# Kernel optimization log

Hardware: AMD Instinct MI355X
Metric: run time of the kernel (lower is better)

The kernel has to match this reference:

```python
import jax, jax.numpy as jnp
from jax import lax
import numpy as np

B, H, W, C = 4, 64, 64, 128
L = H * W
DI = 2 * C   # mamba d_inner (expand=2)
NS = 16      # d_state
R = C // 16  # dt_rank
K = 4        # d_conv
S = 4        # scan branches: fwd, bwd, extra1, extra2


def setup_inputs():
    key = jax.random.key(0)
    ks = jax.random.split(key, 20)
    g = lambda i, shape, s=0.02: jax.random.normal(ks[i], shape, jnp.float32) * s
    return {
        "I1": jax.random.normal(ks[0], (B, L, C), jnp.float32),
        "fusion_resi": jax.random.normal(ks[1], (B, L, C), jnp.float32),
        "I2": jax.random.normal(ks[2], (B, L, C), jnp.float32),
        "fusion": jax.random.normal(ks[3], (B, L, C), jnp.float32),
        "ln1_w": jnp.ones((C,)), "ln1_b": jnp.zeros((C,)),
        "ln2_w": jnp.ones((C,)), "ln2_b": jnp.zeros((C,)),
        "ln3_w": jnp.ones((C,)), "ln3_b": jnp.zeros((C,)),
        "sp_w": g(4, (1, 2, 5, 5), 0.1),
        "ca_w1": g(5, (C // 4, C), 0.05),
        "ca_w2": g(6, (C, C // 4), 0.05),
        "dw_w": g(7, (C, 1, 3, 3), 0.1),
        "dw_b": jnp.zeros((C,)),
        "in_proj_w": g(8, (2 * DI, C)),
        "in_proj1_w": g(9, (DI, C)),
        "in_proj2_w": g(10, (DI, C)),
        "conv_w": g(11, (S, DI, K), 0.1),
        "conv_b": jnp.zeros((S, DI)),
        "xproj_w": g(12, (S, R + 2 * NS, DI)),
        "dt_w": g(13, (S, DI, R), 0.1),
        "dt_b": jnp.full((S, DI), -4.6, jnp.float32),  # softplus -> dt ~ 0.01
        "A_log": jnp.broadcast_to(jnp.log(jnp.arange(1, NS + 1, dtype=jnp.float32)), (S, DI, NS)) * 1.0,
        "Dskip": jnp.ones((S, DI)),
        "out_w": g(14, (C, DI)),
        "test_h": H, "test_w": W,
    }


def ln(x, w, b):
    mu = x.mean(-1, keepdims=True)
    xc = x - mu
    v = (xc * xc).mean(-1, keepdims=True)
    return xc / jnp.sqrt(v + 1e-5) * w + b


def sp_att(x, w, h, wd):
    # x: (B, N, C) -> (B, N, 1) spatial attention map
    Bb = x.shape[0]
    m = jnp.concatenate([x.mean(2, keepdims=True), x.max(2, keepdims=True)], 2)
    m = m.transpose(0, 2, 1).reshape(Bb, 2, h, wd)
    o = lax.conv_general_dilated(m, w, (1, 1), [(2, 2), (2, 2)],
                                 dimension_numbers=("NCHW", "OIHW", "NCHW"))
    return jax.nn.sigmoid(o).reshape(Bb, 1, -1).transpose(0, 2, 1)


def mamba_m3(xf, e1, e2, in_proj_w, in_proj1_w, in_proj2_w, conv_w, conv_b,
             xproj_w, dt_w, dt_b, A_log, Dskip, out_w):
    Bb, Ll, _ = xf.shape
    xz = xf @ in_proj_w.T                       # (B,L,2DI)
    x, z = xz[..., :DI], xz[..., DI:]
    # 4 branches: forward, backward (flipped), extra_emb1, extra_emb2
    u = jnp.stack([x, x[:, ::-1], e1 @ in_proj1_w.T, e2 @ in_proj2_w.T], 0)  # (S,B,L,DI)

    def causal_dwconv(xb, w, b):                # xb (B,L,DI)
        xp = jnp.pad(xb.transpose(0, 2, 1), ((0, 0), (0, 0), (K - 1, 0)))
        o = lax.conv_general_dilated(xp, w[:, None, :], (1,), "VALID",
                                     feature_group_count=DI,
                                     dimension_numbers=("NCH", "OIH", "NCH"))
        return (o + b[None, :, None]).transpose(0, 2, 1)

    uc = jax.nn.silu(jax.vmap(causal_dwconv)(u, conv_w, conv_b))        # (S,B,L,DI)
    proj = jnp.einsum("sbld,spd->sblp", uc, xproj_w)
    dt = jax.nn.softplus(jnp.einsum("sblr,sdr->sbld", proj[..., :R], dt_w)
                         + dt_b[:, None, None, :])                      # (S,B,L,DI)
    Bm, Cm = proj[..., R:R + NS], proj[..., R + NS:]                    # (S,B,L,NS)
    A = -jnp.exp(A_log)                                                 # (S,DI,NS)

    def step(h, inp):
        dt_t, B_t, C_t, u_t = inp                                       # (S,B,DI),(S,B,NS),(S,B,NS),(S,B,DI)
        dA = jnp.exp(dt_t[..., None] * A[:, None])                      # (S,B,DI,NS)
        h = h * dA + (dt_t * u_t)[..., None] * B_t[:, :, None, :]
        return h, jnp.einsum("sbdn,sbn->sbd", h, C_t)

    xs = tuple(t.transpose(2, 0, 1, 3) for t in (dt, Bm, Cm, uc))
    h0 = jnp.zeros((S, Bb, DI, NS), xf.dtype)
    _, ys = lax.scan(step, h0, xs)                                      # (L,S,B,DI)
    y = ys.transpose(1, 2, 0, 3) + uc * Dskip[:, None, None, :]         # (S,B,L,DI)
    y_tot = y[0] + y[1][:, ::-1] + y[2] + y[3]
    return (y_tot * jax.nn.silu(z)) @ out_w.T


def reference(I1, fusion_resi, I2, fusion, ln1_w, ln1_b, ln2_w, ln2_b, ln3_w,
              ln3_b, sp_w, ca_w1, ca_w2, dw_w, dw_b, in_proj_w, in_proj1_w,
              in_proj2_w, conv_w, conv_b, xproj_w, dt_w, dt_b, A_log, Dskip,
              out_w, test_h, test_w):
    fusion_resi = fusion + fusion_resi
    fusion = ln(fusion_resi, ln1_w, ln1_b)
    I2 = ln(I2 * sp_att(I2, sp_w, test_h, test_w), ln2_w, ln2_b)
    I1 = ln(I1 * sp_att(I1, sp_w, test_h, test_w), ln3_w, ln3_b)
    # note: original applies norm1/norm2/norm3 a second time here (faithful)
    gf = mamba_m3(ln(fusion, ln1_w, ln1_b), ln(I2, ln2_w, ln2_b),
                  ln(I1, ln3_w, ln3_b), in_proj_w, in_proj1_w, in_proj2_w,
                  conv_w, conv_b, xproj_w, dt_w, dt_b, A_log, Dskip, out_w)
    Bb, _, Cc = gf.shape
    f4 = gf.transpose(0, 2, 1).reshape(Bb, Cc, test_h, test_w)
    # ChannelAttention1 (already returns x*sig) then extra *fusion per source
    fc = lambda v: jnp.maximum(v @ ca_w1.T, 0.0) @ ca_w2.T
    sig = jax.nn.sigmoid(fc(f4.mean((2, 3))) + fc(f4.max((2, 3))))[:, :, None, None]
    f4 = (f4 * sig) * f4
    dw = lax.conv_general_dilated(f4, dw_w, (1, 1), [(1, 1), (1, 1)],
                                  feature_group_count=Cc,
                                  dimension_numbers=("NCHW", "OIHW", "NCHW"))
    dw = dw + dw_b[None, :, None, None]
    out = (dw + f4).reshape(Bb, Cc, -1).transpose(0, 2, 1)
    return out, fusion_resi
```

## Files before the change

kernel.cpp:

```cpp
#include <hip/hip_runtime.h>

#define DEVI __device__ __forceinline__

static constexpr int BB=4, CC=128, LLn=4096, DI=256, NS=16, RR=8, SS=4;
static constexpr int PP = RR + 2*NS;
static constexpr int CT = 32, NCH = LLn/CT;
static constexpr int NCHF = 64;
static constexpr size_t BLC  = (size_t)BB*LLn*CC;
static constexpr size_t BLD  = (size_t)BB*LLn*DI;
static constexpr size_t SBLD = (size_t)SS*BLD;
static constexpr size_t SBLP = (size_t)SS*BB*LLn*PP;

static constexpr int OW_LN1W=0, OW_LN1B=128, OW_LN2W=256, OW_LN2B=384, OW_LN3W=512, OW_LN3B=640,
 OW_SPW=768, OW_CAW1=820, OW_CAW2=4916, OW_DWW=9012, OW_DWB=10164, OW_IPW=10292,
 OW_IP1W=75828, OW_IP2W=108596, OW_CVW=141364, OW_CVB=145460, OW_XPW=146484,
 OW_DTW=187444, OW_DTB=195636, OW_ALOG=196660, OW_DSK=213044, OW_OUTW=214068;
static constexpr int NW_RAW = 246836;
static constexpr int NW_END = 246848;

__constant__ int c_woff[22] = {OW_LN1W,OW_LN1B,OW_LN2W,OW_LN2B,OW_LN3W,OW_LN3B,OW_SPW,OW_CAW1,
 OW_CAW2,OW_DWW,OW_DWB,OW_IPW,OW_IP1W,OW_IP2W,OW_CVW,OW_CVB,OW_XPW,OW_DTW,OW_DTB,OW_ALOG,
 OW_DSK,OW_OUTW};
__constant__ int c_wsz[22]  = {128,128,128,128,128,128,50,4096,4096,1152,128,65536,32768,32768,
 4096,1024,40960,8192,1024,16384,1024,32768};

static constexpr size_t O_XF   = NW_END;
static constexpr size_t O_E1   = O_XF + BLC;
static constexpr size_t O_E2   = O_E1 + BLC;
static constexpr size_t O_Z    = O_E2 + BLC;
static constexpr size_t O_U    = O_Z + BLD;
static constexpr size_t O_UC   = O_U + SBLD;
static constexpr size_t O_PROJ = O_UC + SBLD;
static constexpr size_t O_SDT  = O_PROJ + SBLP;
static constexpr size_t O_H    = O_SDT + (size_t)SS*BB*NCHF*DI;
static constexpr size_t O_M    = O_H + (size_t)SS*BB*NCHF*DI*NS;
static constexpr size_t O_S    = O_M + 2*(size_t)BB*2*LLn;
static constexpr size_t O_GF   = O_S + 2*(size_t)BB*LLn;
static constexpr size_t O_PART = O_GF + BLC;
static constexpr size_t O_SIG  = O_PART + 2*(size_t)BB*32*CC;
static constexpr size_t WS_END = O_SIG + (size_t)BB*CC;

typedef __attribute__((ext_vector_type(8))) short short8v;
typedef __attribute__((ext_vector_type(4))) float f32x4;

DEVI float bfu2f(unsigned short s){ union{unsigned u; float f;} c; c.u = ((unsigned)s)<<16; return c.f; }
DEVI unsigned short f2bfu(float f){ union{float f; unsigned u;} c; c.f=f;
  unsigned r = c.u + 0x7FFFu + ((c.u>>16)&1u); return (unsigned short)(r>>16); }
DEVI float4 bf4(uint2 v){ return make_float4(bfu2f((unsigned short)(v.x&0xFFFFu)), bfu2f((unsigned short)(v.x>>16)),
                                             bfu2f((unsigned short)(v.y&0xFFFFu)), bfu2f((unsigned short)(v.y>>16))); }
DEVI uint2 pk4(float4 v){ uint2 p;
  p.x = (unsigned)f2bfu(v.x) | ((unsigned)f2bfu(v.y)<<16);
  p.y = (unsigned)f2bfu(v.z) | ((unsigned)f2bfu(v.w)<<16); return p; }
DEVI bool bfmode(const void* ln1w){ return *(const unsigned*)ln1w == 0x3F803F80u; }
DEVI float2 ldin2(const void* p, int i, bool isbf){
  if(isbf){ unsigned v = *(const unsigned*)((const unsigned short*)p + i);
    return make_float2(bfu2f((unsigned short)(v & 0xFFFFu)), bfu2f((unsigned short)(v >> 16))); }
  const float* f = (const float*)p + i; return make_float2(f[0], f[1]);
}
DEVI float wsum(float v){
#pragma unroll
  for(int o=32;o;o>>=1) v += __shfl_xor(v,o,64);
  return v; }
DEVI float wmaxr(float v){
#pragma unroll
  for(int o=32;o;o>>=1) v = fmaxf(v, __shfl_xor(v,o,64));
  return v; }
DEVI float sigf(float x){ return 1.f/(1.f+__expf(-x)); }
DEVI float2 ln_wave(float2 x, const float* Wf, int ow, int ob, int lane){
  float mu = wsum(x.x + x.y) * (1.f/(float)CC);
  float dx = x.x - mu, dy = x.y - mu;
  float var = wsum(dx*dx + dy*dy) * (1.f/(float)CC);
  float rs = rsqrtf(var + 1e-5f);
  int c = 2*lane;
  return make_float2(dx*rs*Wf[ow+c] + Wf[ob+c], dy*rs*Wf[ow+c+1] + Wf[ob+c+1]);
}

struct Srcs { const void* p[22]; };

__global__ void k_xwpad(unsigned* __restrict__ xw32){
  int i = blockIdx.x*256 + threadIdx.x;
  xw32[i] = 0u;
}

__global__ void k_wcvt(Srcs s, float* __restrict__ ws,
                       unsigned short* __restrict__ wip, unsigned short* __restrict__ wob,
                       unsigned short* __restrict__ xw){
  bool isbf = bfmode(s.p[0]);
  int idx = blockIdx.x*256 + threadIdx.x;
  if(idx >= NW_RAW) return;
  int t = 0;
  while(t < 21 && idx >= c_woff[t+1]) t++;
  int j = idx - c_woff[t];
  if(j >= c_wsz[t]) return;
  float v = isbf ? bfu2f(((const unsigned short*)s.p[t])[j]) : ((const float*)s.p[t])[j];
  ws[idx] = v;
  if(t==11)      wip[j]         = f2bfu(v);
  else if(t==12) wip[65536+j]   = f2bfu(v);
  else if(t==13) wip[98304+j]   = f2bfu(v);
  else if(t==21) wob[j]         = f2bfu(v);
  else if(t==16){
    int sid = j / 10240, rem = j % 10240;
    xw[((size_t)sid*64 + rem/256)*256 + (rem%256)] = f2bfu(v);
  }
}

__global__ void k_fuse(const void* fus, const void* fres, const void* ln1raw,
                       float* __restrict__ ws, float* __restrict__ outf,
                       unsigned short* __restrict__ xbf){
  bool isbf = bfmode(ln1raw);
  int lane = threadIdx.x & 63, wv = threadIdx.x >> 6;
  int row = blockIdx.x*4 + wv;
  int base = row*CC;
  float2 a = ldin2(fus, base+2*lane, isbf);
  float2 b = ldin2(fres, base+2*lane, isbf);
  float2 fr = make_float2(a.x+b.x, a.y+b.y);
  *(float2*)(outf + BLC + base + 2*lane) = fr;
  float2 y = ln_wave(fr, ws, OW_LN1W, OW_LN1B, lane);
  y = ln_wave(y, ws, OW_LN1W, OW_LN1B, lane);
  unsigned pk = (unsigned)f2bfu(y.x) | ((unsigned)f2bfu(y.y)<<16);
  *(unsigned*)&xbf[base + 2*lane] = pk;
}

__global__ void k_meanmax(const void* I1, const void* I2, const void* ln1raw, float* __restrict__ ws){
  bool isbf = bfmode(ln1raw);
  int lane = threadIdx.x & 63, wv = threadIdx.x >> 6;
  int g = blockIdx.x*4 + wv;
  int ten = g & 1, row = g >> 1;
  const void* src = ten ? I2 : I1;
  float2 x = ldin2(src, row*CC + 2*lane, isbf);
  float sm = wsum(x.x + x.y) * (1.f/(float)CC);
  float mx = wmaxr(fmaxf(x.x, x.y));
  if(lane == 0){
    int b = row >> 12, l = row & 4095;
    float* mt = ws + O_M + (size_t)ten*(BB*2*LLn);
    mt[(size_t)b*2*LLn + l] = sm;
    mt[(size_t)b*2*LLn + LLn + l] = mx;
  }
}

__global__ void k_spconv(float* __restrict__ ws){
  int idx = blockIdx.x*256 + threadIdx.x;
  int ten = idx >> 14, b = (idx>>12)&3, l = idx & 4095;
  int h = l >> 6, w = l & 63;
  const float* mt = ws + O_M + (size_t)ten*(BB*2*LLn) + (size_t)b*2*LLn;
  float acc = 0.f;
  for(int ci=0; ci<2; ci++)
    for(int kh=0; kh<5; kh++){
      int hh = h + kh - 2; if((unsigned)hh >= 64u) continue;
      for(int kw=0; kw<5; kw++){
        int wn = w + kw - 2; if((unsigned)wn >= 64u) continue;
        acc += mt[(size_t)ci*LLn + hh*64 + wn] * ws[OW_SPW + ci*25 + kh*5 + kw];
      }
    }
  ws[O_S + (size_t)ten*(BB*LLn) + (size_t)b*LLn + l] = sigf(acc);
}

__global__ void k_escale(const void* I1, const void* I2, const void* ln1raw,
                         float* __restrict__ ws, unsigned short* __restrict__ xbf){
  bool isbf = bfmode(ln1raw);
  int lane = threadIdx.x & 63, wv = threadIdx.x >> 6;
  int g = blockIdx.x*4 + wv;
  int ten = g & 1, row = g >> 1;
  const void* src = ten ? I1 : I2;
  float sc = ws[O_S + (ten ? 0 : (size_t)BB*LLn) + row];
  float2 x = ldin2(src, row*CC + 2*lane, isbf);
  x.x *= sc; x.y *= sc;
  int ow = ten ? OW_LN3W : OW_LN2W, ob = ten ? OW_LN3B : OW_LN2B;
  float2 y = ln_wave(x, ws, ow, ob, lane);
  y = ln_wave(y, ws, ow, ob, lane);
  unsigned short* eb = xbf + (ten ? 2*BLC : BLC);
  unsigned pk = (unsigned)f2bfu(y.x) | ((unsigned)f2bfu(y.y)<<16);
  *(unsigned*)&eb[row*CC + 2*lane] = pk;
}

__global__ __launch_bounds__(256) void k_gemm_bf(const unsigned short* __restrict__ Abf,
    const unsigned short* __restrict__ Wbf, float* __restrict__ out,
    int Kd, int N, int mode, unsigned short* __restrict__ ub16, float* __restrict__ z){
  __shared__ unsigned short As[64*64];
  __shared__ unsigned short Bs[64*64];
  const int tid = threadIdx.x, lane = tid & 63, w = tid >> 6;
  const int n0 = blockIdx.x*64, m0 = blockIdx.y*64;
  const int g = lane >> 4, rlo = lane & 15;
  if(mode == 2) Wbf += (size_t)(m0 >> 14) * (64*256);
  f32x4 acc[4];
#pragma unroll
  for(int i=0;i<4;i++) acc[i] = (f32x4){0.f,0.f,0.f,0.f};
  const int nk = Kd >> 6;
  for(int kt=0; kt<nk; kt++){
#pragma unroll
    for(int it=0; it<2; it++){
      int idx = it*256 + tid, r = idx>>3, c = idx&7;
      uint4 av = *(const uint4*)&Abf[(size_t)(m0+r)*Kd + kt*64 + c*8];
      uint4 bv = *(const uint4*)&Wbf[(size_t)(n0+r)*Kd + kt*64 + c*8];
      int sw = (c*16) ^ ((r&7)<<4);
      *(uint4*)((char*)As + r*128 + sw) = av;
      *(uint4*)((char*)Bs + r*128 + sw) = bv;
    }
    __syncthreads();
#pragma unroll
    for(int ks=0; ks<2; ks++){
      int kb = ks*64 + g*16;
      int brow = w*16 + rlo;
      short8v bf = *(short8v*)((char*)Bs + brow*128 + (kb ^ ((rlo&7)<<4)));
#pragma unroll
      for(int rt=0; rt<4; rt++){
        int arow = rt*16 + rlo;
        short8v af = *(short8v*)((char*)As + arow*128 + (kb ^ ((rlo&7)<<4)));
        acc[rt] = __builtin_amdgcn_mfma_f32_16x16x32_bf16(af, bf, acc[rt], 0, 0, 0);
      }
    }
    __syncthreads();
  }
#pragma unroll
  for(int rt=0; rt<4; rt++){
#pragma unroll
    for(int j=0; j<4; j++){
      int m = m0 + rt*16 + g*4 + j;
      int n = n0 + w*16 + rlo;
      float val = acc[rt][j];
      if(mode == 1){
        int b = m >> 12, l = m & (LLn-1);
        if(n < DI) ub16[((size_t)b*LLn + l)*DI + n] = f2bfu(val);
        else       z[((size_t)b*LLn + l)*DI + (n-DI)] = val;
      } else if(mode == 3){
        ub16[(size_t)m*N + n] = f2bfu(val);
      } else {
        if(n < N) out[(size_t)m*N + n] = val;
      }
    }
  }
}

__global__ void k_conv(const float* __restrict__ ws, const unsigned short* __restrict__ ubf,
                       unsigned short* __restrict__ ucbf){
  int t = blockIdx.x*256 + threadIdx.x;
  int dg = t & 63, lg = (t>>6) & 1023, sb = t >> 16, s = sb >> 2, b = sb & 3;
  int d0 = dg*4, l0 = lg*4;
  float wv[16];
  const float* wp = ws + OW_CVW + ((size_t)s*DI + d0)*4;
#pragma unroll
  for(int q=0;q<16;q++) wv[q] = wp[q];
  float4 cb = *(const float4*)&ws[OW_CVB + s*DI + d0];
  const bool rev = (s == 1);
  const unsigned short* ub = ubf + (rev ? (size_t)b*LLn : (size_t)sb*LLn)*DI;
  float4 w0, w1, w2;
  {
    int lm;
    lm = l0-3; w0 = (lm<0)?make_float4(0,0,0,0):bf4(*(const uint2*)&ub[(size_t)(rev?(LLn-1-lm):lm)*DI + d0]);
    lm = l0-2; w1 = (lm<0)?make_float4(0,0,0,0):bf4(*(const uint2*)&ub[(size_t)(rev?(LLn-1-lm):lm)*DI + d0]);
    lm = l0-1; w2 = (lm<0)?make_float4(0,0,0,0):bf4(*(const uint2*)&ub[(size_t)(rev?(LLn-1-lm):lm)*DI + d0]);
  }
#pragma unroll
  for(int r=0;r<4;r++){
    int l = l0 + r;
    float4 w3 = bf4(*(const uint2*)&ub[(size_t)(rev?(LLn-1-l):l)*DI + d0]);
    float4 acc;
    acc.x = cb.x + wv[0]*w0.x + wv[1]*w1.x + wv[2]*w2.x + wv[3]*w3.x;
    acc.y = cb.y + wv[4]*w0.y + wv[5]*w1.y + wv[6]*w2.y + wv[7]*w3.y;
    acc.z = cb.z + wv[8]*w0.z + wv[9]*w1.z + wv[10]*w2.z + wv[11]*w3.z;
    acc.w = cb.w + wv[12]*w0.w + wv[13]*w1.w + wv[14]*w2.w + wv[15]*w3.w;
    acc.x *= sigf(acc.x); acc.y *= sigf(acc.y); acc.z *= sigf(acc.z); acc.w *= sigf(acc.w);
    ushort4 o4; o4.x=f2bfu(acc.x); o4.y=f2bfu(acc.y); o4.z=f2bfu(acc.z); o4.w=f2bfu(acc.w);
    *(ushort4*)&ucbf[((size_t)sb*LLn + l)*DI + d0] = o4;
    w0 = w1; w1 = w2; w2 = w3;
  }
}

template<bool PH3>
__global__ __launch_bounds__(256) void k_scan(float* __restrict__ ws,
                                              const unsigned short* __restrict__ ucbf){
  __shared__ float pl[CT*PP];
  int ch = blockIdx.x & (NCH-1), sb = blockIdx.x >> 7, s = sb >> 2;
  int d = threadIdx.x;
  size_t prow = ((size_t)sb*LLn + (size_t)ch*CT)*PP;
#pragma unroll
  for(int i=0;i<5;i++){ int idx = i*256 + threadIdx.x; pl[idx] = ws[O_PROJ + prow + idx]; }
  __syncthreads();
  unsigned short* ybf = (unsigned short*)(ws + O_U);
  unsigned short* Hb  = (unsigned short*)(ws + O_H);
  unsigned short* Sdb = (unsigned short*)(ws + O_SDT);
  float4 dtw0 = *(const float4*)&ws[OW_DTW + ((size_t)s*DI + d)*RR];
  float4 dtw1 = *(const float4*)&ws[OW_DTW + ((size_t)s*DI + d)*RR + 4];
  float dtb = ws[OW_DTB + s*DI + d];
  float an2[NS]; bool fast = true;
#pragma unroll
  for(int n=0;n<NS;n++){
    float a = -__expf(ws[OW_ALOG + ((size_t)s*DI + d)*NS + n]);
    an2[n] = a * 1.44269504f;
    fast = fast && (fabsf(a + (float)(n+1)) < 1e-4f);
  }
  float4 h0,h1,h2,h3;
  size_t hb = (((size_t)sb*NCH + ch)*DI + d)*NS;
  if(PH3){
    uint4 ha = *(const uint4*)&Hb[hb];
    uint4 hc = *(const uint4*)&Hb[hb+8];
    h0 = bf4(make_uint2(ha.x,ha.y)); h1 = bf4(make_uint2(ha.z,ha.w));
    h2 = bf4(make_uint2(hc.x,hc.y)); h3 = bf4(make_uint2(hc.z,hc.w));
  } else {
    h0=h1=h2=h3=make_float4(0.f,0.f,0.f,0.f);
  }
  float dsk = PH3 ? ws[OW_DSK + s*DI + d] : 0.f;
  float sdt = 0.f;
  size_t ub = ((size_t)sb*LLn + (size_t)ch*CT)*DI + d;
  if(fast){
    for(int ll=0; ll<CT; ll++){
      const float* pr = &pl[ll*PP];
      float4 p0 = *(const float4*)pr, p1 = *(const float4*)(pr+4);
      float x = dtb + p0.x*dtw0.x + p0.y*dtw0.y + p0.z*dtw0.z + p0.w*dtw0.w
                    + p1.x*dtw1.x + p1.y*dtw1.y + p1.z*dtw1.z + p1.w*dtw1.w;
      float dt = (x > 15.f) ? x : __logf(1.f + __expf(x));
      float ut = bfu2f(ucbf[ub + (size_t)ll*DI]);
      float du = dt*ut;
      float e = __expf(-dt);
      float e2 = e*e, e4 = e2*e2;
      float4 da = make_float4(e, e2, e2*e, e4);
      float4 B0 = *(const float4*)(pr+8),  B1 = *(const float4*)(pr+12),
             B2 = *(const float4*)(pr+16), B3 = *(const float4*)(pr+20);
      if(PH3){
        float4 C0 = *(const float4*)(pr+24), C1 = *(const float4*)(pr+28),
               C2 = *(const float4*)(pr+32), C3 = *(const float4*)(pr+36);
        float y;
        h0.x = fmaf(h0.x, da.x, du*B0.x); y  = h0.x*C0.x;
        h0.y = fmaf(h0.y, da.y, du*B0.y); y = fmaf(h0.y, C0.y, y);
        h0.z = fmaf(h0.z, da.z, du*B0.z); y = fmaf(h0.z, C0.z, y);
        h0.w = fmaf(h0.w, da.w, du*B0.w); y = fmaf(h0.w, C0.w, y);
        da.x *= e4; da.y *= e4; da.z *= e4; da.w *= e4;
        h1.x = fmaf(h1.x, da.x, du*B1.x); y = fmaf(h1.x, C1.x, y);
        h1.y = fmaf(h1.y, da.y, du*B1.y); y = fmaf(h1.y, C1.y, y);
        h1.z = fmaf(h1.z, da.z, du*B1.z); y = fmaf(h1.z, C1.z, y);
        h1.w = fmaf(h1.w, da.w, du*B1.w); y = fmaf(h1.w, C1.w, y);
        da.x *= e4; da.y *= e4; da.z *= e4; da.w *= e4;
        h2.x = fmaf(h2.x, da.x, du*B2.x); y = fmaf(h2.x, C2.x, y);
        h2.y = fmaf(h2.y, da.y, du*B2.y); y = fmaf(h2.y, C2.y, y);
        h2.z = fmaf(h2.z, da.z, du*B2.z); y = fmaf(h2.z, C2.z, y);
        h2.w = fmaf(h2.w, da.w, du*B2.w); y = fmaf(h2.w, C2.w, y);
        da.x *= e4; da.y *= e4; da.z *= e4; da.w *= e4;
        h3.x = fmaf(h3.x, da.x, du*B3.x); y = fmaf(h3.x, C3.x, y);
        h3.y = fmaf(h3.y, da.y, du*B3.y); y = fmaf(h3.y, C3.y, y);
        h3.z = fmaf(h3.z, da.z, du*B3.z); y = fmaf(h3.z, C3.z, y);
        h3.w = fmaf(h3.w, da.w, du*B3.w); y = fmaf(h3.w, C3.w, y);
        ybf[ub + (size_t)ll*DI] = f2bfu(y + ut*dsk);
      } else {
        h0.x = fmaf(h0.x, da.x, du*B0.x); h0.y = fmaf(h0.y, da.y, du*B0.y);
        h0.z = fmaf(h0.z, da.z, du*B0.z); h0.w = fmaf(h0.w, da.w, du*B0.w);
        da.x *= e4; da.y *= e4; da.z *= e4; da.w *= e4;
        h1.x = fmaf(h1.x, da.x, du*B1.x); h1.y = fmaf(h1.y, da.y, du*B1.y);
        h1.z = fmaf(h1.z, da.z, du*B1.z); h1.w = fmaf(h1.w, da.w, du*B1.w);
        da.x *= e4; da.y *= e4; da.z *= e4; da.w *= e4;
        h2.x = fmaf(h2.x, da.x, du*B2.x); h2.y = fmaf(h2.y, da.y, du*B2.y);
        h2.z = fmaf(h2.z, da.z, du*B2.z); h2.w = fmaf(h2.w, da.w, du*B2.w);
        da.x *= e4; da.y *= e4; da.z *= e4; da.w *= e4;
        h3.x = fmaf(h3.x, da.x, du*B3.x); h3.y = fmaf(h3.y, da.y, du*B3.y);
        h3.z = fmaf(h3.z, da.z, du*B3.z); h3.w = fmaf(h3.w, da.w, du*B3.w);
        sdt += dt;
      }
    }
  } else {
    float h[NS];
    h[0]=h0.x;h[1]=h0.y;h[2]=h0.z;h[3]=h0.w; h[4]=h1.x;h[5]=h1.y;h[6]=h1.z;h[7]=h1.w;
    h[8]=h2.x;h[9]=h2.y;h[10]=h2.z;h[11]=h2.w; h[12]=h3.x;h[13]=h3.y;h[14]=h3.z;h[15]=h3.w;
    for(int ll=0; ll<CT; ll++){
      const float* pr = &pl[ll*PP];
      float x = dtb;
      x += pr[0]*dtw0.x + pr[1]*dtw0.y + pr[2]*dtw0.z + pr[3]*dtw0.w;
      x += pr[4]*dtw1.x + pr[5]*dtw1.y + pr[6]*dtw1.z + pr[7]*dtw1.w;
      float dt = (x > 15.f) ? x : __logf(1.f + __expf(x));
      float ut = bfu2f(ucbf[ub + (size_t)ll*DI]);
      float du = dt*ut;
      if(PH3){
        float y = 0.f;
#pragma unroll
        for(int n=0;n<NS;n++){ float da = exp2f(an2[n]*dt); h[n] = h[n]*da + du*pr[RR+n]; y += h[n]*pr[RR+NS+n]; }
        ybf[ub + (size_t)ll*DI] = f2bfu(y + ut*dsk);
      } else {
#pragma unroll
        for(int n=0;n<NS;n++){ float da = exp2f(an2[n]*dt); h[n] = h[n]*da + du*pr[RR+n]; }
        sdt += dt;
      }
    }
    h0=make_float4(h[0],h[1],h[2],h[3]); h1=make_float4(h[4],h[5],h[6],h[7]);
    h2=make_float4(h[8],h[9],h[10],h[11]); h3=make_float4(h[12],h[13],h[14],h[15]);
  }
  if(!PH3){
    uint2 a = pk4(h0), b2 = pk4(h1), c = pk4(h2), dd = pk4(h3);
    *(uint4*)&Hb[hb]   = make_uint4(a.x,a.y,b2.x,b2.y);
    *(uint4*)&Hb[hb+8] = make_uint4(c.x,c.y,dd.x,dd.y);
    Sdb[((size_t)sb*NCH + ch)*DI + d] = f2bfu(sdt);
  }
}

__global__ void k_scan2(float* __restrict__ ws){
  int t = blockIdx.x*256 + threadIdx.x;
  int n = t & (NS-1), d = (t>>4) & (DI-1), sb = t >> 12, s = sb >> 2;
  float an2 = -__expf(ws[OW_ALOG + ((size_t)s*DI + d)*NS + n]) * 1.44269504f;
  float hin = 0.f;
  unsigned short* Hb  = (unsigned short*)(ws + O_H);
  const unsigned short* Sdb = (const unsigned short*)(ws + O_SDT);
  for(int c=0;c<NCH;c++){
    size_t hi = (((size_t)sb*NCH + c)*DI + d)*NS + n;
    float he = bfu2f(Hb[hi]);
    float sd = bfu2f(Sdb[((size_t)sb*NCH + c)*DI + d]);
    Hb[hi] = f2bfu(hin);
    hin = he + exp2f(an2*sd)*hin;
  }
}

__global__ void k_gate(float* __restrict__ ws, unsigned short* __restrict__ gbf){
  int t = blockIdx.x*256 + threadIdx.x;
  int d4 = t & 63, l = (t>>6)&4095, b = t>>18;
  int d0 = d4*4;
  const unsigned short* ybf = (const unsigned short*)(ws + O_U);
  size_t i0 = ((size_t)(0*BB+b)*LLn + l)*DI + d0;
  size_t i1 = ((size_t)(1*BB+b)*LLn + (LLn-1-l))*DI + d0;
  size_t i2 = ((size_t)(2*BB+b)*LLn + l)*DI + d0;
  size_t i3 = ((size_t)(3*BB+b)*LLn + l)*DI + d0;
  float4 a = bf4(*(const uint2*)&ybf[i0]);
  float4 bb4 = bf4(*(const uint2*)&ybf[i1]);
  float4 c = bf4(*(const uint2*)&ybf[i2]);
  float4 dd = bf4(*(const uint2*)&ybf[i3]);
  size_t zi = ((size_t)b*LLn + l)*DI + d0;
  float4 zv = *(const float4*)&ws[O_Z + zi];
  float4 g;
  g.x = (a.x+bb4.x+c.x+dd.x) * (zv.x*sigf(zv.x));
  g.y = (a.y+bb4.y+c.y+dd.y) * (zv.y*sigf(zv.y));
  g.z = (a.z+bb4.z+c.z+dd.z) * (zv.z*sigf(zv.z));
  g.w = (a.w+bb4.w+c.w+dd.w) * (zv.w*sigf(zv.w));
  *(uint2*)&gbf[zi] = pk4(g);
}

__global__ void k_redmm(float* __restrict__ ws){
  int b = blockIdx.x >> 5, seg = blockIdx.x & 31, c = threadIdx.x;
  const float* gf = ws + O_GF;
  float sm = 0.f, mx = -3e38f;
  size_t base = ((size_t)b*LLn + (size_t)seg*128)*CC + c;
  for(int i=0;i<128;i++){ float v = gf[base + (size_t)i*CC]; sm += v; mx = fmaxf(mx, v); }
  ws[O_PART + ((size_t)b*32 + seg)*CC + c] = sm;
  ws[O_PART + (size_t)BB*32*CC + ((size_t)b*32 + seg)*CC + c] = mx;
}

__global__ void k_catt(float* __restrict__ ws){
  __shared__ float vm[CC], vx[CC], hm[32], hx[32];
  int b = blockIdx.x, c = threadIdx.x;
  float sm = 0.f, mx = -3e38f;
  for(int seg=0;seg<32;seg++){
    sm += ws[O_PART + ((size_t)b*32+seg)*CC + c];
    mx = fmaxf(mx, ws[O_PART + (size_t)BB*32*CC + ((size_t)b*32+seg)*CC + c]);
  }
  vm[c] = sm * (1.f/(float)LLn); vx[c] = mx;
  __syncthreads();
  if(c < 32){
    float am = 0.f, ax = 0.f;
    for(int k=0;k<CC;k++){ float w1 = ws[OW_CAW1 + c*CC + k]; am += vm[k]*w1; ax += vx[k]*w1; }
    hm[c] = fmaxf(am, 0.f); hx[c] = fmaxf(ax, 0.f);
  }
  __syncthreads();
  float om = 0.f, ox = 0.f;
  for(int k=0;k<32;k++){ float w2 = ws[OW_CAW2 + c*32 + k]; om += hm[k]*w2; ox += hx[k]*w2; }
  ws[O_SIG + (size_t)b*CC + c] = sigf(om + ox);
}

__global__ void k_final(float* __restrict__ ws, float* __restrict__ outf){
  int t = blockIdx.x*256 + threadIdx.x;
  int c4 = t & 31, l = (t>>5)&4095, b = t>>17;
  int h = l>>6, w = l&63;
  const float* gf = ws + O_GF;
  float4 sg = *(const float4*)&ws[O_SIG + (size_t)b*CC + c4*4];
  size_t rb = ((size_t)b*LLn)*CC;
  float4 gc = *(const float4*)&gf[rb + (size_t)l*CC + c4*4];
  float4 fc = make_float4(gc.x*gc.x*sg.x, gc.y*gc.y*sg.y, gc.z*gc.z*sg.z, gc.w*gc.w*sg.w);
  float4 acc = *(const float4*)&ws[OW_DWB + c4*4];
  float wv[4][9];
#pragma unroll
  for(int j=0;j<4;j++)
#pragma unroll
    for(int q=0;q<9;q++) wv[j][q] = ws[OW_DWW + (c4*4+j)*9 + q];
#pragma unroll
  for(int kh=0;kh<3;kh++){
    int hh = h + kh - 1; if((unsigned)hh >= 64u) continue;
#pragma unroll
    for(int kw=0;kw<3;kw++){
      int wn = w + kw - 1; if((unsigned)wn >= 64u) continue;
      float4 g = *(const float4*)&gf[rb + (size_t)(hh*64+wn)*CC + c4*4];
      int q = kh*3+kw;
      acc.x += wv[0][q]*g.x*g.x*sg.x;
      acc.y += wv[1][q]*g.y*g.y*sg.y;
      acc.z += wv[2][q]*g.z*g.z*sg.z;
      acc.w += wv[3][q]*g.w*g.w*sg.w;
    }
  }
  float4 o = make_float4(acc.x+fc.x, acc.y+fc.y, acc.z+fc.z, acc.w+fc.w);
  size_t ob = ((size_t)b*LLn + l)*CC + c4*4;
  *(float4*)&outf[ob] = o;
}

extern "C" void kernel_launch(void* const* d_in, const int* in_sizes, int n_in,
                              void* d_out, int out_size, void* d_ws, size_t ws_size,
                              hipStream_t stream){
  (void)in_sizes; (void)n_in; (void)out_size;
  if(ws_size < WS_END*sizeof(float)) return;
  float* ws = (float*)d_ws;
  float* outf = (float*)d_out;
  const void* I1 = d_in[0]; const void* FRES = d_in[1];
  const void* I2 = d_in[2]; const void* FUS  = d_in[3];
  const void* LN1RAW = d_in[4];

  unsigned short* xbf   = (unsigned short*)(ws + O_H);
  unsigned short* gbf   = xbf;
  unsigned short* wipbf = (unsigned short*)(ws + O_GF);
  unsigned short* wobf  = (unsigned short*)(ws + O_PART);
  unsigned short* xwbf  = (unsigned short*)(ws + O_XF);
  unsigned short* ucbf  = (unsigned short*)(ws + O_UC);
  unsigned short* ubf   = (unsigned short*)(ws + O_U);

  Srcs sr;
  for(int i=0;i<22;i++) sr.p[i] = d_in[4+i];
  k_xwpad<<<128, 256, 0, stream>>>((unsigned*)xwbf);
  k_wcvt<<<(NW_RAW+255)/256, 256, 0, stream>>>(sr, ws, wipbf, wobf, xwbf);
  k_fuse<<<4096, 256, 0, stream>>>(FUS, FRES, LN1RAW, ws, outf, xbf);
  k_meanmax<<<8192, 256, 0, stream>>>(I1, I2, LN1RAW, ws);
  k_spconv<<<128, 256, 0, stream>>>(ws);
  k_escale<<<8192, 256, 0, stream>>>(I1, I2, LN1RAW, ws, xbf);
  k_gemm_bf<<<dim3(8,256), 256, 0, stream>>>(xbf,         wipbf,       nullptr,      128, 512, 1, ubf,        ws+O_Z);
  k_gemm_bf<<<dim3(4,256), 256, 0, stream>>>(xbf+BLC,     wipbf+65536, nullptr,      128, 256, 3, ubf+2*BLD,  nullptr);
  k_gemm_bf<<<dim3(4,256), 256, 0, stream>>>(xbf+2*BLC,   wipbf+98304, nullptr,      128, 256, 3, ubf+3*BLD,  nullptr);
  k_conv<<<4096, 256, 0, stream>>>(ws, ubf, ucbf);
  k_gemm_bf<<<dim3(1,1024), 256, 0, stream>>>(ucbf, xwbf, ws+O_PROJ, 256, 40, 2, nullptr, nullptr);
  k_scan<false><<<SS*BB*NCH, 256, 0, stream>>>(ws, ucbf);
  k_scan2<<<256, 256, 0, stream>>>(ws);
  k_scan<true><<<SS*BB*NCH, 256, 0, stream>>>(ws, ucbf);
  k_gate<<<4096, 256, 0, stream>>>(ws, gbf);
  k_gemm_bf<<<dim3(2,256), 256, 0, stream>>>(gbf, wobf, ws+O_GF, 256, 128, 0, nullptr, nullptr);
  k_redmm<<<128, 128, 0, stream>>>(ws);
  k_catt<<<4, 128, 0, stream>>>(ws);
  k_final<<<2048, 256, 0, stream>>>(ws, outf);
}
```

Measured before the change: 250.2 us.

## Fuse depthwise conv+SiLU into x_proj GEMM and parallelize chunk-carry scan with shuffles

The causal depthwise conv and SiLU are now computed inside the x_proj GEMM's tile-loading stage. Each tile is written to ucbf and staged straight into shared memory for the MFMA, which removes a separate kernel launch and one read of the conv output. The serial 128-step inter-chunk state propagation is replaced by a per-wave parallel prefix scan over the linear recurrence using shuffles, in two 64-chunk halves with a carry between them. This raises parallelism from 65k serial threads to many waves, but the conv work is recomputed with 4x overlapping reads per row inside the GEMM.

```diff
diff --git a/kernel.cpp b/kernel.cpp
--- a/kernel.cpp
+++ b/kernel.cpp
@@ -181,7 +181,6 @@
   const int tid = threadIdx.x, lane = tid & 63, w = tid >> 6;
   const int n0 = blockIdx.x*64, m0 = blockIdx.y*64;
   const int g = lane >> 4, rlo = lane & 15;
-  if(mode == 2) Wbf += (size_t)(m0 >> 14) * (64*256);
   f32x4 acc[4];
 #pragma unroll
   for(int i=0;i<4;i++) acc[i] = (f32x4){0.f,0.f,0.f,0.f};
@@ -231,38 +230,95 @@
   }
 }
 
-__global__ void k_conv(const float* __restrict__ ws, const unsigned short* __restrict__ ubf,
-                       unsigned short* __restrict__ ucbf){
-  int t = blockIdx.x*256 + threadIdx.x;
-  int dg = t & 63, lg = (t>>6) & 1023, sb = t >> 16, s = sb >> 2, b = sb & 3;
-  int d0 = dg*4, l0 = lg*4;
-  float wv[16];
-  const float* wp = ws + OW_CVW + ((size_t)s*DI + d0)*4;
-#pragma unroll
-  for(int q=0;q<16;q++) wv[q] = wp[q];
-  float4 cb = *(const float4*)&ws[OW_CVB + s*DI + d0];
+__global__ __launch_bounds__(256) void k_cxgemm(const float* __restrict__ ws,
+    const unsigned short* __restrict__ ubf, unsigned short* __restrict__ ucbf,
+    const unsigned short* __restrict__ xwbf, float* __restrict__ out){
+  __shared__ unsigned short As[64*64];
+  __shared__ unsigned short Bs[64*64];
+  __shared__ float cwl[DI*4 + DI];
+  const int tid = threadIdx.x, lane = tid & 63, w = tid >> 6;
+  const int m0 = blockIdx.y*64;
+  const int sb = m0 >> 12, s = sb >> 2, b = sb & 3, l0 = m0 & 4095;
+  const int g = lane >> 4, rlo = lane & 15;
   const bool rev = (s == 1);
   const unsigned short* ub = ubf + (rev ? (size_t)b*LLn : (size_t)sb*LLn)*DI;
-  float4 w0, w1, w2;
-  {
-    int lm;
-    lm = l0-3; w0 = (lm<0)?make_float4(0,0,0,0):bf4(*(const uint2*)&ub[(size_t)(rev?(LLn-1-lm):lm)*DI + d0]);
-    lm = l0-2; w1 = (lm<0)?make_float4(0,0,0,0):bf4(*(const uint2*)&ub[(size_t)(rev?(LLn-1-lm):lm)*DI + d0]);
-    lm = l0-1; w2 = (lm<0)?make_float4(0,0,0,0):bf4(*(const uint2*)&ub[(size_t)(rev?(LLn-1-lm):lm)*DI + d0]);
-  }
-#pragma unroll
-  for(int r=0;r<4;r++){
-    int l = l0 + r;
-    float4 w3 = bf4(*(const uint2*)&ub[(size_t)(rev?(LLn-1-l):l)*DI + d0]);
-    float4 acc;
-    acc.x = cb.x + wv[0]*w0.x + wv[1]*w1.x + wv[2]*w2.x + wv[3]*w3.x;
-    acc.y = cb.y + wv[4]*w0.y + wv[5]*w1.y + wv[6]*w2.y + wv[7]*w3.y;
-    acc.z = cb.z + wv[8]*w0.z + wv[9]*w1.z + wv[10]*w2.z + wv[11]*w3.z;
-    acc.w = cb.w + wv[12]*w0.w + wv[13]*w1.w + wv[14]*w2.w + wv[15]*w3.w;
-    acc.x *= sigf(acc.x); acc.y *= sigf(acc.y); acc.z *= sigf(acc.z); acc.w *= sigf(acc.w);
-    ushort4 o4; o4.x=f2bfu(acc.x); o4.y=f2bfu(acc.y); o4.z=f2bfu(acc.z); o4.w=f2bfu(acc.w);
-    *(ushort4*)&ucbf[((size_t)sb*LLn + l)*DI + d0] = o4;
-    w0 = w1; w1 = w2; w2 = w3;
+  const unsigned short* Wbf = xwbf + (size_t)s*(64*256);
+#pragma unroll
+  for(int i=0;i<5;i++){
+    int idx = i*256 + tid;
+    if(idx < DI*4)      cwl[idx] = ws[OW_CVW + (size_t)s*DI*4 + idx];
+    else if(idx < DI*5) cwl[idx] = ws[OW_CVB + s*DI + (idx - DI*4)];
+  }
+  __syncthreads();
+  f32x4 acc[4];
+#pragma unroll
+  for(int i=0;i<4;i++) acc[i] = (f32x4){0.f,0.f,0.f,0.f};
+#pragma unroll
+  for(int kt=0; kt<4; kt++){
+#pragma unroll
+    for(int it=0; it<2; it++){
+      int idx = it*256 + tid, r = idx>>3, c = idx&7;
+      int ch0 = kt*64 + c*8;
+      int l = l0 + r;
+      float4 ulo[4], uhi[4];
+#pragma unroll
+      for(int k=0;k<4;k++){
+        int lm = l - 3 + k;
+        if(lm < 0){ ulo[k]=make_float4(0,0,0,0); uhi[k]=make_float4(0,0,0,0); }
+        else {
+          uint4 uv = *(const uint4*)&ub[(size_t)(rev?(LLn-1-lm):lm)*DI + ch0];
+          ulo[k] = bf4(make_uint2(uv.x,uv.y)); uhi[k] = bf4(make_uint2(uv.z,uv.w));
+        }
+      }
+      float res[8];
+#pragma unroll
+      for(int j=0;j<4;j++){
+        const float* cw = &cwl[(ch0+j)*4];
+        float a = cwl[DI*4 + ch0 + j];
+        float v0 = (&ulo[0].x)[j], v1 = (&ulo[1].x)[j], v2 = (&ulo[2].x)[j], v3 = (&ulo[3].x)[j];
+        a += cw[0]*v0 + cw[1]*v1 + cw[2]*v2 + cw[3]*v3;
+        res[j] = a * sigf(a);
+      }
+#pragma unroll
+      for(int j=0;j<4;j++){
+        const float* cw = &cwl[(ch0+4+j)*4];
+        float a = cwl[DI*4 + ch0 + 4 + j];
+        float v0 = (&uhi[0].x)[j], v1 = (&uhi[1].x)[j], v2 = (&uhi[2].x)[j], v3 = (&uhi[3].x)[j];
+        a += cw[0]*v0 + cw[1]*v1 + cw[2]*v2 + cw[3]*v3;
+        res[4+j] = a * sigf(a);
+      }
+      uint2 plo = pk4(make_float4(res[0],res[1],res[2],res[3]));
+      uint2 phi = pk4(make_float4(res[4],res[5],res[6],res[7]));
+      uint4 pk = make_uint4(plo.x, plo.y, phi.x, phi.y);
+      *(uint4*)&ucbf[((size_t)sb*LLn + l)*DI + ch0] = pk;
+      int sw = (c*16) ^ ((r&7)<<4);
+      *(uint4*)((char*)As + r*128 + sw) = pk;
+      uint4 bv = *(const uint4*)&Wbf[(size_t)r*256 + kt*64 + c*8];
+      *(uint4*)((char*)Bs + r*128 + sw) = bv;
+    }
+    __syncthreads();
+#pragma unroll
+    for(int ks=0; ks<2; ks++){
+      int kb = ks*64 + g*16;
+      int brow = w*16 + rlo;
+      short8v bf = *(short8v*)((char*)Bs + brow*128 + (kb ^ ((rlo&7)<<4)));
+#pragma unroll
+      for(int rt=0; rt<4; rt++){
+        int arow = rt*16 + rlo;
+        short8v af = *(short8v*)((char*)As + arow*128 + (kb ^ ((rlo&7)<<4)));
+        acc[rt] = __builtin_amdgcn_mfma_f32_16x16x32_bf16(af, bf, acc[rt], 0, 0, 0);
+      }
+    }
+    __syncthreads();
+  }
+#pragma unroll
+  for(int rt=0; rt<4; rt++){
+#pragma unroll
+    for(int j=0; j<4; j++){
+      int m = m0 + rt*16 + g*4 + j;
+      int n = w*16 + rlo;
+      if(n < PP) out[(size_t)m*PP + n] = acc[rt][j];
+    }
   }
 }
 
@@ -389,20 +445,41 @@
   }
 }
 
-__global__ void k_scan2(float* __restrict__ ws){
-  int t = blockIdx.x*256 + threadIdx.x;
-  int n = t & (NS-1), d = (t>>4) & (DI-1), sb = t >> 12, s = sb >> 2;
+__global__ __launch_bounds__(256) void k_scan2w(float* __restrict__ ws){
+  int wid = blockIdx.x*4 + (threadIdx.x >> 6);
+  int lane = threadIdx.x & 63;
+  int sb = wid >> 12, rem = wid & 4095, d = rem >> 4, n = rem & 15, s = sb >> 2;
   float an2 = -__expf(ws[OW_ALOG + ((size_t)s*DI + d)*NS + n]) * 1.44269504f;
-  float hin = 0.f;
   unsigned short* Hb  = (unsigned short*)(ws + O_H);
   const unsigned short* Sdb = (const unsigned short*)(ws + O_SDT);
-  for(int c=0;c<NCH;c++){
-    size_t hi = (((size_t)sb*NCH + c)*DI + d)*NS + n;
-    float he = bfu2f(Hb[hi]);
-    float sd = bfu2f(Sdb[((size_t)sb*NCH + c)*DI + d]);
-    Hb[hi] = f2bfu(hin);
-    hin = he + exp2f(an2*sd)*hin;
-  }
+  size_t hi = (((size_t)sb*NCH + lane)*DI + d)*NS + n;
+  size_t si = ((size_t)sb*NCH + lane)*DI + d;
+  float a = bfu2f(Hb[hi]);
+  float bcoef = exp2f(an2 * bfu2f(Sdb[si]));
+#pragma unroll
+  for(int off=1; off<64; off<<=1){
+    float ap = __shfl_up(a, off, 64);
+    float bp = __shfl_up(bcoef, off, 64);
+    if(lane >= off){ a = fmaf(bcoef, ap, a); bcoef *= bp; }
+  }
+  float hin = __shfl_up(a, 1, 64);
+  if(lane == 0) hin = 0.f;
+  float carry = __shfl(a, 63, 64);
+  Hb[hi] = f2bfu(hin);
+  size_t hi2 = hi + (size_t)64*DI*NS;
+  size_t si2 = si + (size_t)64*DI;
+  float a2 = bfu2f(Hb[hi2]);
+  float b2 = exp2f(an2 * bfu2f(Sdb[si2]));
+#pragma unroll
+  for(int off=1; off<64; off<<=1){
+    float ap = __shfl_up(a2, off, 64);
+    float bp = __shfl_up(b2, off, 64);
+    if(lane >= off){ a2 = fmaf(b2, ap, a2); b2 *= bp; }
+  }
+  float a2p = __shfl_up(a2, 1, 64);
+  float b2p = __shfl_up(b2, 1, 64);
+  float hin2 = (lane == 0) ? carry : fmaf(b2p, carry, a2p);
+  Hb[hi2] = f2bfu(hin2);
 }
 
 __global__ void k_gate(float* __restrict__ ws, unsigned short* __restrict__ gbf){
@@ -523,10 +600,9 @@
   k_gemm_bf<<<dim3(8,256), 256, 0, stream>>>(xbf,         wipbf,       nullptr,      128, 512, 1, ubf,        ws+O_Z);
   k_gemm_bf<<<dim3(4,256), 256, 0, stream>>>(xbf+BLC,     wipbf+65536, nullptr,      128, 256, 3, ubf+2*BLD,  nullptr);
   k_gemm_bf<<<dim3(4,256), 256, 0, stream>>>(xbf+2*BLC,   wipbf+98304, nullptr,      128, 256, 3, ubf+3*BLD,  nullptr);
-  k_conv<<<4096, 256, 0, stream>>>(ws, ubf, ucbf);
-  k_gemm_bf<<<dim3(1,1024), 256, 0, stream>>>(ucbf, xwbf, ws+O_PROJ, 256, 40, 2, nullptr, nullptr);
+  k_cxgemm<<<dim3(1,1024), 256, 0, stream>>>(ws, ubf, ucbf, xwbf, ws+O_PROJ);
   k_scan<false><<<SS*BB*NCH, 256, 0, stream>>>(ws, ucbf);
-  k_scan2<<<256, 256, 0, stream>>>(ws);
+  k_scan2w<<<16384, 256, 0, stream>>>(ws);
   k_scan<true><<<SS*BB*NCH, 256, 0, stream>>>(ws, ucbf);
   k_gate<<<4096, 256, 0, stream>>>(ws, gbf);
   k_gemm_bf<<<dim3(2,256), 256, 0, stream>>>(gbf, wobf, ws+O_GF, 256, 128, 0, nullptr, nullptr);
```

New measurement: 304.9 us. 21.9% more time.
